# Kernel optimization log

Hardware: AMD Instinct MI355X
Metric: run time of the kernel (lower is better)

The kernel has to match this reference:

```python
import jax, jax.numpy as jnp
import numpy as np

IN_CH = 256
OUT_CH = 64
HEADS = 8


def setup_inputs() -> dict:
    key = jax.random.key(0)
    ks = jax.random.split(key, 7)
    N = 4096
    proj = OUT_CH * HEADS
    s_in = 1.0 / np.sqrt(IN_CH)
    return {
        "query_input": jax.random.normal(ks[0], (N, IN_CH), dtype=jnp.float32),
        "Wq": jax.random.uniform(ks[1], (proj, IN_CH), jnp.float32, -s_in, s_in),
        "bq": jax.random.uniform(ks[2], (proj,), jnp.float32, -s_in, s_in),
        "Wk": jax.random.uniform(ks[3], (proj, IN_CH), jnp.float32, -s_in, s_in),
        "bk": jax.random.uniform(ks[4], (proj,), jnp.float32, -s_in, s_in),
        "Wv": jax.random.uniform(ks[5], (proj, IN_CH), jnp.float32, -s_in, s_in),
        "bv": jax.random.uniform(ks[6], (proj,), jnp.float32, -s_in, s_in),
    }


def reference(query_input, Wq, bq, Wk, bk, Wv, bv):
    N = query_input.shape[0]
    # projections -> [N, H, M]
    q = (query_input @ Wq.T + bq).reshape(N, HEADS, OUT_CH)
    k = (query_input @ Wk.T + bk).reshape(N, HEADS, OUT_CH)
    v = (query_input @ Wv.T + bv).reshape(N, HEADS, OUT_CH)
    # sigmoid attention scores [N, L, H]
    attention_num = jax.nn.sigmoid(jnp.einsum('nhm,lhm->nlh', q, k))
    # sum-normalization over L (keys)
    normalizer = attention_num.sum(axis=1, keepdims=True)  # [N, 1, H]
    attention = attention_num / normalizer
    # weighted V reduction [N, H, D], then mean over heads -> [N, D]
    out = jnp.einsum('nlh,lhd->nhd', attention, v).mean(axis=1)
    return out
```

## Files before the change

kernel.cpp:

```cpp
#include <hip/hip_runtime.h>
#include <hip/hip_bf16.h>
#include <math.h>

#define N_TOK 4096
#define IN_CH 256
#define OUT_CH 64
#define HEADS 8
#define PROJ (OUT_CH * HEADS)
#define NLOG2E -1.44269504088896340736f

typedef float f32x4 __attribute__((ext_vector_type(4)));
typedef float f32x16 __attribute__((ext_vector_type(16)));
typedef __bf16 bf16x8 __attribute__((ext_vector_type(8)));
typedef unsigned short ushort_t;

__device__ inline ushort_t bf16rne(float x) {
    unsigned u = __float_as_uint(x);
    unsigned r = (u + 0x7FFFu + ((u >> 16) & 1u)) >> 16;
    return (ushort_t)r;
}

__global__ __launch_bounds__(256) void cast_pack_kernel(
    const float* __restrict__ X,
    const float* __restrict__ Wq, const float* __restrict__ Wk,
    const float* __restrict__ Wv,
    ushort_t* __restrict__ Xa, ushort_t* __restrict__ Wp)
{
    const int i = blockIdx.x * 256 + threadIdx.x;
    const float* src;
    ushort_t* dst;
    float scale = 1.0f;
    if (i < 131072) {
        const int t = i & 15, quad = (i >> 4) & 3, k8 = (i >> 6) & 7, g = i >> 9;
        src = X + (size_t)(g * 16 + t) * IN_CH + k8 * 32 + quad * 8;
        dst = Xa + (size_t)i * 8;
    } else {
        const int j = i - 131072;
        const int z = j >> 14;
        const int r = j & 16383;
        const int cl = r & 15, quad = (r >> 4) & 3, k8 = (r >> 6) & 7, gc = r >> 9;
        const float* W = (z == 0) ? Wq : (z == 1) ? Wk : Wv;
        src = W + (size_t)(gc * 16 + cl) * IN_CH + k8 * 32 + quad * 8;
        dst = Wp + (size_t)z * 131072 * 8 + (size_t)r * 8;
        if (z == 0) scale = NLOG2E;
    }
    float4 a = *(const float4*)src;
    float4 b = *(const float4*)(src + 4);
    ushort_t pk[8];
    pk[0] = bf16rne(a.x * scale); pk[1] = bf16rne(a.y * scale);
    pk[2] = bf16rne(a.z * scale); pk[3] = bf16rne(a.w * scale);
    pk[4] = bf16rne(b.x * scale); pk[5] = bf16rne(b.y * scale);
    pk[6] = bf16rne(b.z * scale); pk[7] = bf16rne(b.w * scale);
    *(uint4*)dst = *(uint4*)pk;
}

__global__ __launch_bounds__(256) void proj_mfma_kernel(
    const ushort_t* __restrict__ Xa, const ushort_t* __restrict__ Wp,
    const float* __restrict__ bq, const float* __restrict__ bk,
    const float* __restrict__ bv,
    ushort_t* __restrict__ Qb, ushort_t* __restrict__ Kb,
    ushort_t* __restrict__ Vt)
{
    const int z = blockIdx.z;
    const float* bias = (z == 0) ? bq : (z == 1) ? bk : bv;
    const float bscale = (z == 0) ? NLOG2E : 1.0f;
    const int c0 = blockIdx.x * 64;
    const int n0 = blockIdx.y * 64;

    const int tid = threadIdx.x;
    const int w = tid >> 6;
    const int lane = tid & 63;
    const int l15 = lane & 15;
    const int quad = lane >> 4;

    __shared__ ushort_t Es[64 * 68];

    const ushort_t* xa = Xa + (size_t)(blockIdx.y * 4 + w) * 4096 + quad * 128 + l15 * 8;
    const ushort_t* wp0 = Wp + (size_t)z * 131072 * 8 +
                          (size_t)(blockIdx.x * 4) * 4096 + quad * 128 + l15 * 8;

    f32x4 acc[4] = {{0.f, 0.f, 0.f, 0.f}, {0.f, 0.f, 0.f, 0.f},
                    {0.f, 0.f, 0.f, 0.f}, {0.f, 0.f, 0.f, 0.f}};

#pragma unroll 2
    for (int k8 = 0; k8 < 8; ++k8) {
        bf16x8 a = *(const bf16x8*)(xa + k8 * 512);
#pragma unroll
        for (int f = 0; f < 4; ++f) {
            bf16x8 b = *(const bf16x8*)(wp0 + f * 4096 + k8 * 512);
            acc[f] = __builtin_amdgcn_mfma_f32_16x16x32_bf16(a, b, acc[f], 0, 0, 0);
        }
    }

    if (z < 2) {
#pragma unroll
        for (int f = 0; f < 4; ++f) {
            const float bb = bias[c0 + f * 16 + l15] * bscale;
#pragma unroll
            for (int r = 0; r < 4; ++r)
                Es[(w * 16 + quad * 4 + r) * 68 + f * 16 + l15] = bf16rne(acc[f][r] + bb);
        }
    } else {
#pragma unroll
        for (int f = 0; f < 4; ++f) {
            const float bb = bias[c0 + f * 16 + l15];
#pragma unroll
            for (int r = 0; r < 4; ++r)
                Es[(f * 16 + l15) * 68 + w * 16 + quad * 4 + r] = bf16rne(acc[f][r] + bb);
        }
    }
    __syncthreads();

    const int erow = tid >> 2;
    const int ecol = (tid & 3) * 16;
    uint4 pk0 = *(uint4*)&Es[erow * 68 + ecol];
    uint4 pk1 = *(uint4*)&Es[erow * 68 + ecol + 8];
    if (z < 2) {
        ushort_t* out = z ? Kb : Qb;
        ushort_t* p = &out[(size_t)(n0 + erow) * PROJ + c0 + ecol];
        *(uint4*)p = pk0;
        *(uint4*)(p + 8) = pk1;
    } else {
        ushort_t* p = &Vt[(size_t)(c0 + erow) * N_TOK + n0 + ecol];
        *(uint4*)p = pk0;
        *(uint4*)(p + 8) = pk1;
    }
}

template<int ZS>
__global__ __launch_bounds__(256, 4) void attn_kernel(
    const ushort_t* __restrict__ Qb, const ushort_t* __restrict__ Kb,
    const ushort_t* __restrict__ Vt,
    float* __restrict__ NUM, float* __restrict__ DEN)
{
    constexpr int KEYS = N_TOK / ZS;
    constexpr int TILES = KEYS / 64;

    const int h = blockIdx.y;
    const int z = blockIdx.z;
    const int n0 = blockIdx.x * 128;
    const int tid = threadIdx.x;
    const int w = tid >> 6;
    const int lane = tid & 63;
    const int l31 = lane & 31;
    const int hf = lane >> 5;

    __shared__ ushort_t Ks[64 * 64];
    __shared__ ushort_t Vs[64 * 64];
    __shared__ ushort_t Ps[4][32 * 72];

    bf16x8 qb[4];
    {
        const ushort_t* base = Qb + (size_t)(n0 + w * 32 + l31) * PROJ + h * 64 + hf * 8;
        qb[0] = *(const bf16x8*)(base);
        qb[1] = *(const bf16x8*)(base + 16);
        qb[2] = *(const bf16x8*)(base + 32);
        qb[3] = *(const bf16x8*)(base + 48);
    }

    f32x16 o0 = {};
    f32x16 o1 = {};
    float den = 0.0f;

    const int srow = tid >> 2;
    const int sc2 = (tid & 3) * 2;
    const int sp0 = (sc2 ^ (srow & 7)) * 8;
    const int sp1 = ((sc2 + 1) ^ (srow & 7)) * 8;
    const int xm = l31 & 7;

    const ushort_t* kgp = Kb + (size_t)h * 64 + sc2 * 8 +
                          (size_t)(z * KEYS + srow) * PROJ;
    const ushort_t* vgp = Vt + (size_t)h * 64 * N_TOK + (size_t)srow * N_TOK +
                          sc2 * 8 + z * KEYS;

    uint4 kr0 = ((const uint4*)kgp)[0], kr1 = ((const uint4*)kgp)[1];
    uint4 vr0 = ((const uint4*)vgp)[0], vr1 = ((const uint4*)vgp)[1];

    ushort_t* pw = &Ps[w][l31 * 72];

    for (int lt = 0; lt < TILES; ++lt) {
        __syncthreads();
        *(uint4*)&Ks[srow * 64 + sp0] = kr0;
        *(uint4*)&Ks[srow * 64 + sp1] = kr1;
        *(uint4*)&Vs[srow * 64 + sp0] = vr0;
        *(uint4*)&Vs[srow * 64 + sp1] = vr1;
        __syncthreads();

        if (lt < TILES - 1) {
            kgp += 64 * PROJ;
            vgp += 64;
            kr0 = ((const uint4*)kgp)[0]; kr1 = ((const uint4*)kgp)[1];
            vr0 = ((const uint4*)vgp)[0]; vr1 = ((const uint4*)vgp)[1];
        }

        f32x16 s0 = {};
        f32x16 s1 = {};
        __builtin_amdgcn_s_setprio(1);
#pragma unroll
        for (int ks = 0; ks < 4; ++ks) {
            const int pos = ((ks * 2 + hf) ^ xm) * 8;
            bf16x8 ka0 = *(const bf16x8*)&Ks[l31 * 64 + pos];
            s0 = __builtin_amdgcn_mfma_f32_32x32x16_bf16(ka0, qb[ks], s0, 0, 0, 0);
            bf16x8 ka1 = *(const bf16x8*)&Ks[(32 + l31) * 64 + pos];
            s1 = __builtin_amdgcn_mfma_f32_32x32x16_bf16(ka1, qb[ks], s1, 0, 0, 0);
        }
        __builtin_amdgcn_s_setprio(0);

#pragma unroll
        for (int rq = 0; rq < 4; ++rq) {
            float p0 = __builtin_amdgcn_rcpf(1.0f + __builtin_amdgcn_exp2f(s0[rq * 4 + 0]));
            float p1 = __builtin_amdgcn_rcpf(1.0f + __builtin_amdgcn_exp2f(s0[rq * 4 + 1]));
            float p2 = __builtin_amdgcn_rcpf(1.0f + __builtin_amdgcn_exp2f(s0[rq * 4 + 2]));
            float p3 = __builtin_amdgcn_rcpf(1.0f + __builtin_amdgcn_exp2f(s0[rq * 4 + 3]));
            den += (p0 + p1) + (p2 + p3);
            unsigned u0 = __float_as_uint(p0) + 0x8000u;
            unsigned u1 = __float_as_uint(p1) + 0x8000u;
            unsigned u2 = __float_as_uint(p2) + 0x8000u;
            unsigned u3 = __float_as_uint(p3) + 0x8000u;
            uint2 pk;
            pk.x = __builtin_amdgcn_perm(u1, u0, 0x07060302u);
            pk.y = __builtin_amdgcn_perm(u3, u2, 0x07060302u);
            *(uint2*)&pw[rq * 8 + hf * 4] = pk;
        }
#pragma unroll
        for (int rq = 0; rq < 4; ++rq) {
            float p0 = __builtin_amdgcn_rcpf(1.0f + __builtin_amdgcn_exp2f(s1[rq * 4 + 0]));
            float p1 = __builtin_amdgcn_rcpf(1.0f + __builtin_amdgcn_exp2f(s1[rq * 4 + 1]));
            float p2 = __builtin_amdgcn_rcpf(1.0f + __builtin_amdgcn_exp2f(s1[rq * 4 + 2]));
            float p3 = __builtin_amdgcn_rcpf(1.0f + __builtin_amdgcn_exp2f(s1[rq * 4 + 3]));
            den += (p0 + p1) + (p2 + p3);
            unsigned u0 = __float_as_uint(p0) + 0x8000u;
            unsigned u1 = __float_as_uint(p1) + 0x8000u;
            unsigned u2 = __float_as_uint(p2) + 0x8000u;
            unsigned u3 = __float_as_uint(p3) + 0x8000u;
            uint2 pk;
            pk.x = __builtin_amdgcn_perm(u1, u0, 0x07060302u);
            pk.y = __builtin_amdgcn_perm(u3, u2, 0x07060302u);
            *(uint2*)&pw[32 + rq * 8 + hf * 4] = pk;
        }

        __builtin_amdgcn_s_setprio(1);
#pragma unroll
        for (int ks = 0; ks < 4; ++ks) {
            bf16x8 pa = *(const bf16x8*)&Ps[w][l31 * 72 + ks * 16 + hf * 8];
            const int pos = ((ks * 2 + hf) ^ xm) * 8;
            bf16x8 vb0 = *(const bf16x8*)&Vs[l31 * 64 + pos];
            o0 = __builtin_amdgcn_mfma_f32_32x32x16_bf16(pa, vb0, o0, 0, 0, 0);
            bf16x8 vb1 = *(const bf16x8*)&Vs[(32 + l31) * 64 + pos];
            o1 = __builtin_amdgcn_mfma_f32_32x32x16_bf16(pa, vb1, o1, 0, 0, 0);
        }
        __builtin_amdgcn_s_setprio(0);
    }

#pragma unroll
    for (int rq = 0; rq < 4; ++rq) {
#pragma unroll
        for (int j = 0; j < 4; ++j) {
            const int q = n0 + w * 32 + rq * 8 + hf * 4 + j;
            float* p = &NUM[((size_t)z * N_TOK + q) * PROJ + h * 64 + l31];
            p[0]  = o0[rq * 4 + j];
            p[32] = o1[rq * 4 + j];
        }
    }
    den += __shfl_xor(den, 32);
    if (lane < 32) {
        DEN[((size_t)z * N_TOK + n0 + w * 32 + lane) * HEADS + h] = den;
    }
}

template<int ZS>
__global__ __launch_bounds__(256) void reduce_kernel(
    const float* __restrict__ NUM, const float* __restrict__ DEN,
    float* __restrict__ out)
{
    const int g = blockIdx.x * 256 + threadIdx.x;
    const int n = g >> 6;
    const int d = g & 63;
    float acc = 0.0f;
#pragma unroll
    for (int hh = 0; hh < HEADS; ++hh) {
        float num = 0.0f, dd = 0.0f;
#pragma unroll
        for (int zz = 0; zz < ZS; ++zz) {
            num += NUM[((size_t)zz * N_TOK + n) * PROJ + hh * 64 + d];
            dd  += DEN[((size_t)zz * N_TOK + n) * HEADS + hh];
        }
        acc += num / dd;
    }
    out[g] = acc * 0.125f;
}

extern "C" void kernel_launch(void* const* d_in, const int* in_sizes, int n_in,
                              void* d_out, int out_size, void* d_ws, size_t ws_size,
                              hipStream_t stream) {
    (void)in_sizes; (void)n_in; (void)out_size;
    const float* X  = (const float*)d_in[0];
    const float* Wq = (const float*)d_in[1];
    const float* bq = (const float*)d_in[2];
    const float* Wk = (const float*)d_in[3];
    const float* bk = (const float*)d_in[4];
    const float* Wv = (const float*)d_in[5];
    const float* bv = (const float*)d_in[6];
    float* out = (float*)d_out;

    const size_t NEED4 =
        (size_t)4 * N_TOK * PROJ * 4 + (size_t)4 * N_TOK * HEADS * 4 +
        (size_t)3 * N_TOK * PROJ * 2 + (size_t)N_TOK * IN_CH * 2 +
        (size_t)3 * PROJ * IN_CH * 2;
    const int ZS = (ws_size >= NEED4) ? 4 : 2;

    float* NUM = (float*)d_ws;
    float* DEN = NUM + (size_t)ZS * N_TOK * PROJ;
    ushort_t* Qb = (ushort_t*)(DEN + (size_t)ZS * N_TOK * HEADS);
    ushort_t* Kb = Qb + (size_t)N_TOK * PROJ;
    ushort_t* Vt = Kb + (size_t)N_TOK * PROJ;
    ushort_t* Xa = Vt + (size_t)N_TOK * PROJ;
    ushort_t* Wp = Xa + (size_t)N_TOK * IN_CH;

    cast_pack_kernel<<<dim3(704), 256, 0, stream>>>(X, Wq, Wk, Wv, Xa, Wp);
    proj_mfma_kernel<<<dim3(PROJ / 64, N_TOK / 64, 3), 256, 0, stream>>>(
        Xa, Wp, bq, bk, bv, Qb, Kb, Vt);
    if (ZS == 4) {
        attn_kernel<4><<<dim3(N_TOK / 128, HEADS, 4), 256, 0, stream>>>(
            Qb, Kb, Vt, NUM, DEN);
        reduce_kernel<4><<<dim3(N_TOK * OUT_CH / 256), 256, 0, stream>>>(
            NUM, DEN, out);
    } else {
        attn_kernel<2><<<dim3(N_TOK / 128, HEADS, 2), 256, 0, stream>>>(
            Qb, Kb, Vt, NUM, DEN);
        reduce_kernel<2><<<dim3(N_TOK * OUT_CH / 256), 256, 0, stream>>>(
            NUM, DEN, out);
    }
}
```

Baseline: 145.0 us.

## Double-buffer K/V tiles and keep P in registers via permlane swaps

K and V shared-memory tiles become double-buffered, so each iteration needs one barrier instead of two and the store of the next tile overlaps the current tile's compute. The sigmoid probabilities are no longer staged through a per-wave LDS buffer. They are packed to bf16 with v_cvt_pk_bf16_f32 and rearranged into the MFMA A-operand layout with v_permlane32_swap, which removes the LDS write/read round trip. The cost is double the K/V LDS footprint and more live registers, which may lower occupancy. The bf16 rounding mode also changes from truncate-with-bias to the hardware conversion.

```diff
diff --git a/kernel.cpp b/kernel.cpp
--- a/kernel.cpp
+++ b/kernel.cpp
@@ -19,6 +19,13 @@
     unsigned r = (u + 0x7FFFu + ((u >> 16) & 1u)) >> 16;
     return (ushort_t)r;
 }
+
+__device__ inline unsigned cvtpk_bf16(float lo, float hi) {
+    unsigned d;
+    asm("v_cvt_pk_bf16_f32 %0, %1, %2" : "=v"(d) : "v"(lo), "v"(hi));
+    return d;
+}
+#define PLSWAP(x, y) asm("v_permlane32_swap_b32 %0, %1" : "+v"(x), "+v"(y))
 
 __global__ __launch_bounds__(256) void cast_pack_kernel(
     const float* __restrict__ X,
@@ -145,9 +152,8 @@
     const int l31 = lane & 31;
     const int hf = lane >> 5;
 
-    __shared__ ushort_t Ks[64 * 64];
-    __shared__ ushort_t Vs[64 * 64];
-    __shared__ ushort_t Ps[4][32 * 72];
+    __shared__ ushort_t Ks[2 * 64 * 64];
+    __shared__ ushort_t Vs[2 * 64 * 64];
 
     bf16x8 qb[4];
     {
@@ -175,22 +181,30 @@
 
     uint4 kr0 = ((const uint4*)kgp)[0], kr1 = ((const uint4*)kgp)[1];
     uint4 vr0 = ((const uint4*)vgp)[0], vr1 = ((const uint4*)vgp)[1];
-
-    ushort_t* pw = &Ps[w][l31 * 72];
+    *(uint4*)&Ks[srow * 64 + sp0] = kr0;
+    *(uint4*)&Ks[srow * 64 + sp1] = kr1;
+    *(uint4*)&Vs[srow * 64 + sp0] = vr0;
+    *(uint4*)&Vs[srow * 64 + sp1] = vr1;
+    if (TILES > 1) {
+        kgp += 64 * PROJ; vgp += 64;
+        kr0 = ((const uint4*)kgp)[0]; kr1 = ((const uint4*)kgp)[1];
+        vr0 = ((const uint4*)vgp)[0]; vr1 = ((const uint4*)vgp)[1];
+    }
 
     for (int lt = 0; lt < TILES; ++lt) {
+        const int bo = (lt & 1) << 12;
         __syncthreads();
-        *(uint4*)&Ks[srow * 64 + sp0] = kr0;
-        *(uint4*)&Ks[srow * 64 + sp1] = kr1;
-        *(uint4*)&Vs[srow * 64 + sp0] = vr0;
-        *(uint4*)&Vs[srow * 64 + sp1] = vr1;
-        __syncthreads();
-
-        if (lt < TILES - 1) {
-            kgp += 64 * PROJ;
-            vgp += 64;
-            kr0 = ((const uint4*)kgp)[0]; kr1 = ((const uint4*)kgp)[1];
-            vr0 = ((const uint4*)vgp)[0]; vr1 = ((const uint4*)vgp)[1];
+        if (lt + 1 < TILES) {
+            const int bw = ((lt + 1) & 1) << 12;
+            *(uint4*)&Ks[bw + srow * 64 + sp0] = kr0;
+            *(uint4*)&Ks[bw + srow * 64 + sp1] = kr1;
+            *(uint4*)&Vs[bw + srow * 64 + sp0] = vr0;
+            *(uint4*)&Vs[bw + srow * 64 + sp1] = vr1;
+            if (lt + 2 < TILES) {
+                kgp += 64 * PROJ; vgp += 64;
+                kr0 = ((const uint4*)kgp)[0]; kr1 = ((const uint4*)kgp)[1];
+                vr0 = ((const uint4*)vgp)[0]; vr1 = ((const uint4*)vgp)[1];
+            }
         }
 
         f32x16 s0 = {};
@@ -199,54 +213,64 @@
 #pragma unroll
         for (int ks = 0; ks < 4; ++ks) {
             const int pos = ((ks * 2 + hf) ^ xm) * 8;
-            bf16x8 ka0 = *(const bf16x8*)&Ks[l31 * 64 + pos];
+            bf16x8 ka0 = *(const bf16x8*)&Ks[bo + l31 * 64 + pos];
             s0 = __builtin_amdgcn_mfma_f32_32x32x16_bf16(ka0, qb[ks], s0, 0, 0, 0);
-            bf16x8 ka1 = *(const bf16x8*)&Ks[(32 + l31) * 64 + pos];
+            bf16x8 ka1 = *(const bf16x8*)&Ks[bo + (32 + l31) * 64 + pos];
             s1 = __builtin_amdgcn_mfma_f32_32x32x16_bf16(ka1, qb[ks], s1, 0, 0, 0);
         }
         __builtin_amdgcn_s_setprio(0);
 
-#pragma unroll
-        for (int rq = 0; rq < 4; ++rq) {
-            float p0 = __builtin_amdgcn_rcpf(1.0f + __builtin_amdgcn_exp2f(s0[rq * 4 + 0]));
-            float p1 = __builtin_amdgcn_rcpf(1.0f + __builtin_amdgcn_exp2f(s0[rq * 4 + 1]));
-            float p2 = __builtin_amdgcn_rcpf(1.0f + __builtin_amdgcn_exp2f(s0[rq * 4 + 2]));
-            float p3 = __builtin_amdgcn_rcpf(1.0f + __builtin_amdgcn_exp2f(s0[rq * 4 + 3]));
-            den += (p0 + p1) + (p2 + p3);
-            unsigned u0 = __float_as_uint(p0) + 0x8000u;
-            unsigned u1 = __float_as_uint(p1) + 0x8000u;
-            unsigned u2 = __float_as_uint(p2) + 0x8000u;
-            unsigned u3 = __float_as_uint(p3) + 0x8000u;
-            uint2 pk;
-            pk.x = __builtin_amdgcn_perm(u1, u0, 0x07060302u);
-            pk.y = __builtin_amdgcn_perm(u3, u2, 0x07060302u);
-            *(uint2*)&pw[rq * 8 + hf * 4] = pk;
-        }
-#pragma unroll
-        for (int rq = 0; rq < 4; ++rq) {
-            float p0 = __builtin_amdgcn_rcpf(1.0f + __builtin_amdgcn_exp2f(s1[rq * 4 + 0]));
-            float p1 = __builtin_amdgcn_rcpf(1.0f + __builtin_amdgcn_exp2f(s1[rq * 4 + 1]));
-            float p2 = __builtin_amdgcn_rcpf(1.0f + __builtin_amdgcn_exp2f(s1[rq * 4 + 2]));
-            float p3 = __builtin_amdgcn_rcpf(1.0f + __builtin_amdgcn_exp2f(s1[rq * 4 + 3]));
-            den += (p0 + p1) + (p2 + p3);
-            unsigned u0 = __float_as_uint(p0) + 0x8000u;
-            unsigned u1 = __float_as_uint(p1) + 0x8000u;
-            unsigned u2 = __float_as_uint(p2) + 0x8000u;
-            unsigned u3 = __float_as_uint(p3) + 0x8000u;
-            uint2 pk;
-            pk.x = __builtin_amdgcn_perm(u1, u0, 0x07060302u);
-            pk.y = __builtin_amdgcn_perm(u3, u2, 0x07060302u);
-            *(uint2*)&pw[32 + rq * 8 + hf * 4] = pk;
-        }
+        float p0[16], p1[16];
+#pragma unroll
+        for (int r = 0; r < 16; ++r) {
+            p0[r] = __builtin_amdgcn_rcpf(1.0f + __builtin_amdgcn_exp2f(s0[r]));
+            den += p0[r];
+        }
+#pragma unroll
+        for (int r = 0; r < 16; ++r) {
+            p1[r] = __builtin_amdgcn_rcpf(1.0f + __builtin_amdgcn_exp2f(s1[r]));
+            den += p1[r];
+        }
+        unsigned d00 = cvtpk_bf16(p0[0],  p0[1]);
+        unsigned d01 = cvtpk_bf16(p0[2],  p0[3]);
+        unsigned d10 = cvtpk_bf16(p0[4],  p0[5]);
+        unsigned d11 = cvtpk_bf16(p0[6],  p0[7]);
+        unsigned d20 = cvtpk_bf16(p0[8],  p0[9]);
+        unsigned d21 = cvtpk_bf16(p0[10], p0[11]);
+        unsigned d30 = cvtpk_bf16(p0[12], p0[13]);
+        unsigned d31 = cvtpk_bf16(p0[14], p0[15]);
+        PLSWAP(d00, d10);
+        PLSWAP(d01, d11);
+        PLSWAP(d20, d30);
+        PLSWAP(d21, d31);
+        unsigned e00 = cvtpk_bf16(p1[0],  p1[1]);
+        unsigned e01 = cvtpk_bf16(p1[2],  p1[3]);
+        unsigned e10 = cvtpk_bf16(p1[4],  p1[5]);
+        unsigned e11 = cvtpk_bf16(p1[6],  p1[7]);
+        unsigned e20 = cvtpk_bf16(p1[8],  p1[9]);
+        unsigned e21 = cvtpk_bf16(p1[10], p1[11]);
+        unsigned e30 = cvtpk_bf16(p1[12], p1[13]);
+        unsigned e31 = cvtpk_bf16(p1[14], p1[15]);
+        PLSWAP(e00, e10);
+        PLSWAP(e01, e11);
+        PLSWAP(e20, e30);
+        PLSWAP(e21, e31);
+
+        union { unsigned u[4]; bf16x8 v; } A0, A1, A2, A3;
+        A0.u[0] = d00; A0.u[1] = d01; A0.u[2] = d10; A0.u[3] = d11;
+        A1.u[0] = d20; A1.u[1] = d21; A1.u[2] = d30; A1.u[3] = d31;
+        A2.u[0] = e00; A2.u[1] = e01; A2.u[2] = e10; A2.u[3] = e11;
+        A3.u[0] = e20; A3.u[1] = e21; A3.u[2] = e30; A3.u[3] = e31;
 
         __builtin_amdgcn_s_setprio(1);
 #pragma unroll
         for (int ks = 0; ks < 4; ++ks) {
-            bf16x8 pa = *(const bf16x8*)&Ps[w][l31 * 72 + ks * 16 + hf * 8];
+            const bf16x8 pa = (ks == 0) ? A0.v : (ks == 1) ? A1.v
+                             : (ks == 2) ? A2.v : A3.v;
             const int pos = ((ks * 2 + hf) ^ xm) * 8;
-            bf16x8 vb0 = *(const bf16x8*)&Vs[l31 * 64 + pos];
+            bf16x8 vb0 = *(const bf16x8*)&Vs[bo + l31 * 64 + pos];
             o0 = __builtin_amdgcn_mfma_f32_32x32x16_bf16(pa, vb0, o0, 0, 0, 0);
-            bf16x8 vb1 = *(const bf16x8*)&Vs[(32 + l31) * 64 + pos];
+            bf16x8 vb1 = *(const bf16x8*)&Vs[bo + (32 + l31) * 64 + pos];
             o1 = __builtin_amdgcn_mfma_f32_32x32x16_bf16(pa, vb1, o1, 0, 0, 0);
         }
         __builtin_amdgcn_s_setprio(0);
```

After: 145.8 us. About the same (+0.6%).
